# Performance work log

Measured on AMD Instinct MI355X. Metric: run time of the kernel, lower is better.

The kernel has to match this reference:

```python
import jax, jax.numpy as jnp
import numpy as np

L, B, H, M, D = 2, 4, 8, 4096, 128  # layers, batch, kv heads/partition, max_len, head_dim
SEQ_LEN = 2048  # active bucket size


def setup_inputs() -> dict:
    key = jax.random.key(0)
    ks = jax.random.split(key, 5)
    return {
        "k_caches": jax.random.normal(ks[0], (L, B, H, M, D), dtype=jnp.float32),
        "v_caches": jax.random.normal(ks[1], (L, B, H, M, D), dtype=jnp.float32),
        "latest_k": jax.random.normal(ks[2], (L, B, H, 1, D), dtype=jnp.float32),
        "latest_v": jax.random.normal(ks[3], (L, B, H, 1, D), dtype=jnp.float32),
        "position_ids": jax.random.randint(ks[4], (B, 1), 0, SEQ_LEN),
        "seq_len": SEQ_LEN,
    }


def reference(k_caches, v_caches, latest_k, latest_v, position_ids, seq_len):
    """KVCacheManager.update_cache, token-gen path, right padding.

    For each layer: slice cache[:, :, :seq_len, :], scatter latest_{k,v}
    (shape B,H,1,D) at position_ids along the sequence dim (torch.scatter
    with an expanded (B,1,Q,1) index), then concat the untouched tail
    cache[:, :, seq_len:, :] back on (\_gather_slice_into_kv_cacheline).
    """
    S = int(seq_len)

    def update_layer(cache, latest):  # cache: (B,H,M,D), latest: (B,H,1,D)
        bucket = cache[:, :, :S, :]  # (B,H,S,D)

        def per_batch(c, l, p):  # c: (H,S,D), l: (H,1,D), p: (1,)
            return c.at[:, p, :].set(l)

        bucket = jax.vmap(per_batch)(bucket, latest, position_ids)
        return jnp.concatenate([bucket, cache[:, :, S:, :]], axis=2)

    k_out = jax.vmap(update_layer)(k_caches, latest_k)  # (L,B,H,M,D)
    v_out = jax.vmap(update_layer)(v_caches, latest_v)  # (L,B,H,M,D)
    return jnp.stack([k_out, v_out])  # (2,L,B,H,M,D)
```

## Files before the change

kernel.cpp:

```cpp
#include <hip/hip_runtime.h>


constexpr int Ln = 2, Bn = 4, Hn = 8, Mn = 4096, Dn = 128;
constexpr long N_ELEM  = (long)Ln * Bn * Hn * Mn * Dn;
constexpr long N_VEC   = N_ELEM / 4;
constexpr long TOT_VEC = 2 * N_VEC;

__global__ __launch_bounds__(256) void kv_update_kernel(
    const float4* __restrict__ kc,
    const float4* __restrict__ vc,
    const float4* __restrict__ lk,
    const float4* __restrict__ lv,
    const int*    __restrict__ pos,
    float4*       __restrict__ out)
{
    long i = (long)blockIdx.x * 256 + threadIdx.x;

    int  lane = (int)(i & 31);
    long t    = i >> 5;
    int  m    = (int)(t & (Mn - 1));
    long t2   = t >> 12;
    int  h    = (int)(t2 & (Hn - 1));
    long t3   = t2 >> 3;
    int  b    = (int)(t3 & (Bn - 1));
    long t4   = t3 >> 2;
    int  l    = (int)(t4 & 1);
    int  kv   = (int)(t4 >> 1);

    const float4* src = kv ? vc : kc;
    float4 val = src[i & (N_VEC - 1)];

    int p = pos[b];
    if (m == p) {
        const float4* lsrc = kv ? lv : lk;
        val = lsrc[((l * Bn + b) * Hn + h) * (Dn / 4) + lane];
    }

    out[i] = val;
}

extern "C" void kernel_launch(void* const* d_in, const int* in_sizes, int n_in,
                              void* d_out, int out_size, void* d_ws, size_t ws_size,
                              hipStream_t stream) {
    const float4* kc  = (const float4*)d_in[0];
    const float4* vc  = (const float4*)d_in[1];
    const float4* lk  = (const float4*)d_in[2];
    const float4* lv  = (const float4*)d_in[3];
    const int*    pos = (const int*)d_in[4];
    float4* out = (float4*)d_out;

    const int block = 256;
    const long grid = TOT_VEC / block;
    kv_update_kernel<<<(dim3)(unsigned)grid, block, 0, stream>>>(kc, vc, lk, lv, pos, out);
}
```

Before: 423.9 us.

## Replace fused copy kernel with device memcpy plus tiny scatter kernel

Both caches are now bulk-copied into the output with two device-to-device hipMemcpyAsync calls. A small 16-block kernel then overwrites only the rows at each batch's position with the latest K/V vectors. This drops the per-element index math and compare from the copy path and hands the bulk transfer to the runtime's copy path (blit kernel or SDMA). It adds two extra stream operations, and the copy engine may give lower bandwidth than a tuned kernel.

```diff
diff --git a/kernel.cpp b/kernel.cpp
--- a/kernel.cpp
+++ b/kernel.cpp
@@ -2,54 +2,46 @@
 
 
 constexpr int Ln = 2, Bn = 4, Hn = 8, Mn = 4096, Dn = 128;
-constexpr long N_ELEM  = (long)Ln * Bn * Hn * Mn * Dn;
-constexpr long N_VEC   = N_ELEM / 4;
-constexpr long TOT_VEC = 2 * N_VEC;
+constexpr long N_ELEM = (long)Ln * Bn * Hn * Mn * Dn;
+constexpr size_t CACHE_BYTES = (size_t)N_ELEM * 4;
 
-__global__ __launch_bounds__(256) void kv_update_kernel(
-    const float4* __restrict__ kc,
-    const float4* __restrict__ vc,
+__global__ __launch_bounds__(256) void kv_scatter_kernel(
     const float4* __restrict__ lk,
     const float4* __restrict__ lv,
     const int*    __restrict__ pos,
     float4*       __restrict__ out)
 {
-    long i = (long)blockIdx.x * 256 + threadIdx.x;
+    int j = blockIdx.x * 256 + threadIdx.x;
+    int lane = j & 31;
+    int t    = j >> 5;
+    int h    = t & (Hn - 1);
+    int t2   = t >> 3;
+    int b    = t2 & (Bn - 1);
+    int t3   = t2 >> 2;
+    int l    = t3 & 1;
+    int kv   = t3 >> 1;
 
-    int  lane = (int)(i & 31);
-    long t    = i >> 5;
-    int  m    = (int)(t & (Mn - 1));
-    long t2   = t >> 12;
-    int  h    = (int)(t2 & (Hn - 1));
-    long t3   = t2 >> 3;
-    int  b    = (int)(t3 & (Bn - 1));
-    long t4   = t3 >> 2;
-    int  l    = (int)(t4 & 1);
-    int  kv   = (int)(t4 >> 1);
-
-    const float4* src = kv ? vc : kc;
-    float4 val = src[i & (N_VEC - 1)];
+    const float4* lsrc = kv ? lv : lk;
+    float4 val = lsrc[((l * Bn + b) * Hn + h) * (Dn / 4) + lane];
 
     int p = pos[b];
-    if (m == p) {
-        const float4* lsrc = kv ? lv : lk;
-        val = lsrc[((l * Bn + b) * Hn + h) * (Dn / 4) + lane];
-    }
-
-    out[i] = val;
+    long row = ((((long)kv * Ln + l) * Bn + b) * Hn + h) * Mn + p;
+    out[row * (Dn / 4) + lane] = val;
 }
 
 extern "C" void kernel_launch(void* const* d_in, const int* in_sizes, int n_in,
                               void* d_out, int out_size, void* d_ws, size_t ws_size,
                               hipStream_t stream) {
-    const float4* kc  = (const float4*)d_in[0];
-    const float4* vc  = (const float4*)d_in[1];
+    const void* kc  = d_in[0];
+    const void* vc  = d_in[1];
     const float4* lk  = (const float4*)d_in[2];
     const float4* lv  = (const float4*)d_in[3];
     const int*    pos = (const int*)d_in[4];
-    float4* out = (float4*)d_out;
 
-    const int block = 256;
-    const long grid = TOT_VEC / block;
-    kv_update_kernel<<<(dim3)(unsigned)grid, block, 0, stream>>>(kc, vc, lk, lv, pos, out);
+    char* out = (char*)d_out;
+
+    hipMemcpyAsync(out,               kc, CACHE_BYTES, hipMemcpyDeviceToDevice, stream);
+    hipMemcpyAsync(out + CACHE_BYTES, vc, CACHE_BYTES, hipMemcpyDeviceToDevice, stream);
+
+    kv_scatter_kernel<<<16, 256, 0, stream>>>(lk, lv, pos, (float4*)d_out);
 }
```

After: 436.9 us. 1.03x slower.
